# Optimization experiments

Hardware: AMD Instinct MI355X
Metric: run time of the kernel (lower is better)

## Reference

```python
import jax, jax.numpy as jnp
import numpy as np

B, L, D, N, V = 32, 4096, 128, 5, 128  # batch, seq, embed dim, n-gram order, alphabet size


def setup_inputs() -> dict:
    key = jax.random.key(0)
    k1, k2, k3 = jax.random.split(key, 3)
    x = jax.random.randint(k1, (B, L), 0, V, dtype=jnp.int32)
    emb = jax.random.normal(k2, (V, D), dtype=jnp.float32)
    W = jax.random.normal(k3, (V, D * (N - 1)), dtype=jnp.float32) * 0.05
    b = jnp.zeros((V,), dtype=jnp.float32)
    return {"x": x, "emb": emb, "W": W, "b": b}


def reference(x, emb, W, b):
    n1 = N - 1  # context window size
    x_enc = emb[x]  # (B, L, D) embedding gather
    # enc[:, j, k*D:(k+1)*D] = x_enc[:, j - n1 + k] for j >= n1; zeros for j < n1.
    # Build each slot by right-shifting the embedded sequence by (n1 - k).
    Lcur = x.shape[1]
    parts = [jnp.pad(x_enc, ((0, 0), (n1 - k, 0), (0, 0)))[:, :Lcur] for k in range(n1)]
    enc = jnp.concatenate(parts, axis=-1)  # (B, L, n1*D)
    valid = (jnp.arange(Lcur) >= n1)[None, :, None]
    enc = jnp.where(valid, enc, jnp.zeros((), enc.dtype))
    # linear: logits = enc @ W^T + b  -> (B, L, V)
    logits = jnp.einsum("blf,vf->blv", enc, W) + b
    return logits
```

## Files before the change

kernel.cpp:

```cpp
#include <hip/hip_runtime.h>

constexpr int Bn = 32;
constexpr int Ln = 4096;
constexpr int Dn = 128;
constexpr int Vn = 128;
constexpr int N1 = 4;

typedef float vfloat4 __attribute__((ext_vector_type(4)));

__global__ void build_table_kernel(const float* __restrict__ emb,
                                   const float* __restrict__ W,
                                   const float* __restrict__ bias,
                                   float* __restrict__ T) {
    const int kt = blockIdx.x;
    const int k  = kt >> 7;
    const int t  = kt & 127;
    const int v  = threadIdx.x;

    __shared__ float4 e[Dn / 4];
    if (threadIdx.x < Dn / 4) {
        e[threadIdx.x] = ((const float4*)(emb + t * Dn))[threadIdx.x];
    }
    __syncthreads();

    const float4* w = (const float4*)(W + (size_t)v * (Dn * N1) + k * Dn);
    float acc = (k == 0) ? bias[v] : 0.f;
#pragma unroll
    for (int i = 0; i < Dn / 4; ++i) {
        float4 wv = w[i];
        float4 ev = e[i];
        acc += wv.x * ev.x + wv.y * ev.y + wv.z * ev.z + wv.w * ev.w;
    }
    T[(size_t)(((v >> 5) * N1 + k) * Vn + t) * 32 + (v & 31)] = acc;
}

constexpr int ROWS = N1 * Vn;

__global__ void __launch_bounds__(512, 4)
ngram_logits_kernel(const int* __restrict__ x,
                    const float* __restrict__ T,
                    const float* __restrict__ bias,
                    float* __restrict__ out) {
    __shared__ float lds[ROWS * 32];

    const int q  = blockIdx.x & 3;
    const int pb = blockIdx.x >> 2;

    {
        const float4* src = (const float4*)(T + (size_t)q * (ROWS * 32));
        float4*       dst = (float4*)lds;
#pragma unroll
        for (int it = 0; it < 8; ++it) {
            const int f = it * 512 + threadIdx.x;
            const int r = f >> 3;
            const int c = f & 7;
            dst[r * 8 + (c ^ (r & 7))] = src[f];
        }
    }
    __syncthreads();

    const int vq = threadIdx.x & 7;
    const int gl = threadIdx.x >> 3;
    const vfloat4* lv   = (const vfloat4*)lds;
    vfloat4*       outq = (vfloat4*)out;

#pragma unroll
    for (int it = 0; it < 4; ++it) {
        const int basepos = pb * 1024 + it * 256 + gl * 4;
        vfloat4*  ob      = outq + (size_t)basepos * 32 + q * 8 + vq;

        if ((basepos & (Ln - 1)) == 0) {
            const vfloat4 bv = ((const vfloat4*)bias)[q * 8 + vq];
#pragma unroll
            for (int i = 0; i < 4; ++i)
                __builtin_nontemporal_store(bv, ob + i * 32);
            continue;
        }

        const int4 xa = *(const int4*)(x + basepos - 4);
        const int4 xb = *(const int4*)(x + basepos);
        const int  w[7] = {xa.x, xa.y, xa.z, xa.w, xb.x, xb.y, xb.z};

#pragma unroll
        for (int i = 0; i < 4; ++i) {
            vfloat4 a = lv[(w[i] << 3) + (vq ^ (w[i] & 7))];
#pragma unroll
            for (int k = 1; k < N1; ++k) {
                const int tok = w[i + k];
                a += lv[((k * Vn + tok) << 3) + (vq ^ (tok & 7))];
            }
            __builtin_nontemporal_store(a, ob + i * 32);
        }
    }
}

extern "C" void kernel_launch(void* const* d_in, const int* in_sizes, int n_in,
                              void* d_out, int out_size, void* d_ws, size_t ws_size,
                              hipStream_t stream) {
    const int*   x    = (const int*)d_in[0];
    const float* emb  = (const float*)d_in[1];
    const float* W    = (const float*)d_in[2];
    const float* bias = (const float*)d_in[3];
    float*       out  = (float*)d_out;
    float*       T    = (float*)d_ws;

    build_table_kernel<<<N1 * Vn, Vn, 0, stream>>>(emb, W, bias, T);

    ngram_logits_kernel<<<512, 512, 0, stream>>>(x, T, bias, out);
}
```

Before: 93.11 us.

## Fuse table build into logits kernel, recomputing table slice per block

```diff
diff --git a/kernel.cpp b/kernel.cpp
--- a/kernel.cpp
+++ b/kernel.cpp
@@ -5,72 +5,73 @@
 constexpr int Dn = 128;
 constexpr int Vn = 128;
 constexpr int N1 = 4;
+constexpr int ROWS = N1 * Vn;
 
 typedef float vfloat4 __attribute__((ext_vector_type(4)));
 
-__global__ void build_table_kernel(const float* __restrict__ emb,
-                                   const float* __restrict__ W,
-                                   const float* __restrict__ bias,
-                                   float* __restrict__ T) {
-    const int kt = blockIdx.x;
-    const int k  = kt >> 7;
-    const int t  = kt & 127;
-    const int v  = threadIdx.x;
-
-    __shared__ float4 e[Dn / 4];
-    if (threadIdx.x < Dn / 4) {
-        e[threadIdx.x] = ((const float4*)(emb + t * Dn))[threadIdx.x];
-    }
-    __syncthreads();
-
-    const float4* w = (const float4*)(W + (size_t)v * (Dn * N1) + k * Dn);
-    float acc = (k == 0) ? bias[v] : 0.f;
-#pragma unroll
-    for (int i = 0; i < Dn / 4; ++i) {
-        float4 wv = w[i];
-        float4 ev = e[i];
-        acc += wv.x * ev.x + wv.y * ev.y + wv.z * ev.z + wv.w * ev.w;
-    }
-    T[(size_t)(((v >> 5) * N1 + k) * Vn + t) * 32 + (v & 31)] = acc;
-}
-
-constexpr int ROWS = N1 * Vn;
-
-__global__ void __launch_bounds__(512, 4)
-ngram_logits_kernel(const int* __restrict__ x,
-                    const float* __restrict__ T,
-                    const float* __restrict__ bias,
-                    float* __restrict__ out) {
+__global__ void __launch_bounds__(512, 2)
+fused_ngram_kernel(const int* __restrict__ x,
+                   const float* __restrict__ emb,
+                   const float* __restrict__ W,
+                   const float* __restrict__ bias,
+                   float* __restrict__ out) {
     __shared__ float lds[ROWS * 32];
 
     const int q  = blockIdx.x & 3;
-    const int pb = blockIdx.x >> 2;
+    const int ph = blockIdx.x >> 2;
+
+    const int vq = threadIdx.x & 7;
+    const float4 bias4 = ((const float4*)bias)[q * 8 + vq];
 
     {
-        const float4* src = (const float4*)(T + (size_t)q * (ROWS * 32));
-        float4*       dst = (float4*)lds;
+        const int r0 = threadIdx.x >> 3;
+        const int v0 = q * 32 + vq * 4;
+        const float* Wb = W + (size_t)v0 * (Dn * N1);
+
+        for (int rr = 0; rr < 8; ++rr) {
+            const int r = rr * 64 + r0;
+            const int t = r & 127;
+            const int k = r >> 7;
+            const float4* e  = (const float4*)(emb + (size_t)t * Dn);
+            const float4* w0 = (const float4*)(Wb + 0 * (size_t)(Dn * N1) + k * Dn);
+            const float4* w1 = (const float4*)(Wb + 1 * (size_t)(Dn * N1) + k * Dn);
+            const float4* w2 = (const float4*)(Wb + 2 * (size_t)(Dn * N1) + k * Dn);
+            const float4* w3 = (const float4*)(Wb + 3 * (size_t)(Dn * N1) + k * Dn);
+
+            float4 s0 = {0, 0, 0, 0}, s1 = {0, 0, 0, 0};
+            float4 s2 = {0, 0, 0, 0}, s3 = {0, 0, 0, 0};
 #pragma unroll
-        for (int it = 0; it < 8; ++it) {
-            const int f = it * 512 + threadIdx.x;
-            const int r = f >> 3;
-            const int c = f & 7;
-            dst[r * 8 + (c ^ (r & 7))] = src[f];
+            for (int i = 0; i < 32; ++i) {
+                const float4 ev = e[i];
+                float4 a = w0[i]; s0.x += a.x * ev.x; s0.y += a.y * ev.y; s0.z += a.z * ev.z; s0.w += a.w * ev.w;
+                float4 b = w1[i]; s1.x += b.x * ev.x; s1.y += b.y * ev.y; s1.z += b.z * ev.z; s1.w += b.w * ev.w;
+                float4 c = w2[i]; s2.x += c.x * ev.x; s2.y += c.y * ev.y; s2.z += c.z * ev.z; s2.w += c.w * ev.w;
+                float4 d = w3[i]; s3.x += d.x * ev.x; s3.y += d.y * ev.y; s3.z += d.z * ev.z; s3.w += d.w * ev.w;
+            }
+            float4 acc;
+            acc.x = s0.x + s0.y + s0.z + s0.w;
+            acc.y = s1.x + s1.y + s1.z + s1.w;
+            acc.z = s2.x + s2.y + s2.z + s2.w;
+            acc.w = s3.x + s3.y + s3.z + s3.w;
+            if (k == 0) {
+                acc.x += bias4.x; acc.y += bias4.y; acc.z += bias4.z; acc.w += bias4.w;
+            }
+            ((float4*)lds)[r * 8 + (vq ^ (t & 7))] = acc;
         }
     }
     __syncthreads();
 
-    const int vq = threadIdx.x & 7;
     const int gl = threadIdx.x >> 3;
     const vfloat4* lv   = (const vfloat4*)lds;
     vfloat4*       outq = (vfloat4*)out;
 
 #pragma unroll
-    for (int it = 0; it < 4; ++it) {
-        const int basepos = pb * 1024 + it * 256 + gl * 4;
+    for (int it = 0; it < 8; ++it) {
+        const int basepos = ph * 2048 + it * 256 + gl * 4;
         vfloat4*  ob      = outq + (size_t)basepos * 32 + q * 8 + vq;
 
         if ((basepos & (Ln - 1)) == 0) {
-            const vfloat4 bv = ((const vfloat4*)bias)[q * 8 + vq];
+            const vfloat4 bv = {bias4.x, bias4.y, bias4.z, bias4.w};
 #pragma unroll
             for (int i = 0; i < 4; ++i)
                 __builtin_nontemporal_store(bv, ob + i * 32);
@@ -102,9 +103,6 @@
     const float* W    = (const float*)d_in[2];
     const float* bias = (const float*)d_in[3];
     float*       out  = (float*)d_out;
-    float*       T    = (float*)d_ws;
 
-    build_table_kernel<<<N1 * Vn, Vn, 0, stream>>>(emb, W, bias, T);
-
-    ngram_logits_kernel<<<512, 512, 0, stream>>>(x, T, bias, out);
+    fused_ngram_kernel<<<256, 512, 0, stream>>>(x, emb, W, bias, out);
 }
```

New measurement: 318.0 us. 3.42x slower.
